# Performance work log

Hardware: AMD Instinct MI355X
Metric: run time of the kernel (lower is better)

The kernel has to match this reference:

```python
import jax, jax.numpy as jnp
import numpy as np

B, H, S, D = 1, 16, 4096, 64

def setup_inputs() -> dict:
    key = jax.random.key(0)
    k1, k2, k3 = jax.random.split(key, 3)
    query = jax.random.normal(k1, (B, H, S, D), dtype=jnp.float32)
    key_t = jax.random.normal(k2, (B, H, S, D), dtype=jnp.float32)
    value = jax.random.normal(k3, (B, H, S, D), dtype=jnp.float32)
    attn_mask = jnp.zeros((B, 1, S, S), dtype=jnp.float32)
    return {"query": query, "key": key_t, "value": value, "attn_mask": attn_mask}

def reference(query, key, value, attn_mask):
    d = query.shape[-1]
    # [B,H,S,S] = QK^T / sqrt(d) + mask
    scores = jnp.einsum("bhqd,bhkd->bhqk", query, key) / jnp.sqrt(jnp.float32(d))
    scores = scores + attn_mask
    probs = jax.nn.softmax(scores, axis=-1)
    # dropout_p = 0.0 -> identity
    out = jnp.einsum("bhqk,bhkd->bhqd", probs, value)
    return out
```

## Files before the change

kernel.cpp:

```cpp
#include <hip/hip_runtime.h>
#include <stdint.h>

#define LOG2E  1.44269504088896f
#define QSCALE (0.125f * LOG2E)

typedef float    f32x4_t  __attribute__((ext_vector_type(4)));
typedef float    f32x16_t __attribute__((ext_vector_type(16)));
typedef _Float16 f16x8_t  __attribute__((ext_vector_type(8)));
typedef _Float16 f16x2_t  __attribute__((ext_vector_type(2)));

#if __has_builtin(__builtin_amdgcn_exp2f)
#define EXP2F(x) __builtin_amdgcn_exp2f(x)
#else
#define EXP2F(x) exp2f(x)
#endif

__device__ __forceinline__ float rowsum2(f16x2_t p, float acc) {
#if __has_builtin(__builtin_amdgcn_fdot2)
  return __builtin_amdgcn_fdot2(p, (f16x2_t){(_Float16)1.0f, (_Float16)1.0f}, acc, false);
#else
  return acc + (float)p[0] + (float)p[1];
#endif
}

__global__ void prep_kernel(const float* __restrict__ M, const float* __restrict__ K,
                            const float* __restrict__ V, _Float16* __restrict__ Kh,
                            _Float16* __restrict__ Vth, int* __restrict__ flag) {
  __shared__ __align__(16) _Float16 T[64 * 72];
  const int tid = threadIdx.x;
  const int bid = blockIdx.x;

  {
    const float* p = M + (size_t)bid * 8192 + (size_t)tid * 4;
    unsigned acc = 0;
#pragma unroll
    for (int i = 0; i < 8; ++i) {
      f32x4_t v = *(const f32x4_t*)(p + (size_t)i * 1024);
      acc |= __float_as_uint(v[0]) | __float_as_uint(v[1]) |
             __float_as_uint(v[2]) | __float_as_uint(v[3]);
    }
    if (acc & 0x7fffffffu) atomicOr(flag, 1);
  }

  if (Kh != nullptr) {
    {
      const size_t idx = ((size_t)bid * 256 + tid) * 8;
      f32x4_t a = *(const f32x4_t*)(K + idx);
      f32x4_t b = *(const f32x4_t*)(K + idx + 4);
      union { _Float16 h[8]; uint4 q; } U;
#pragma unroll
      for (int j = 0; j < 4; ++j) { U.h[j] = (_Float16)a[j]; U.h[4 + j] = (_Float16)b[j]; }
      *(uint4*)(Kh + idx) = U.q;
    }
    if (bid < 1024) {
      const int head = bid >> 6;
      const int st   = bid & 63;
      const size_t hoff = (size_t)head * 4096 * 64;
      const int sl    = tid >> 2;
      const int fbase = (tid & 3) * 16;
      const float* src = V + hoff + (size_t)(st * 64 + sl) * 64 + fbase;
#pragma unroll
      for (int c = 0; c < 4; ++c) {
        f32x4_t a = *(const f32x4_t*)(src + c * 4);
#pragma unroll
        for (int j = 0; j < 4; ++j) T[(fbase + c * 4 + j) * 72 + sl] = (_Float16)a[j];
      }
      __syncthreads();
      const int feat = tid >> 2;
      const int sb   = (tid & 3) * 16;
      uint4 r0 = *(const uint4*)&T[feat * 72 + sb];
      uint4 r1 = *(const uint4*)&T[feat * 72 + sb + 8];
      _Float16* dst = Vth + hoff + (size_t)feat * 4096 + st * 64 + sb;
      *(uint4*)(dst)     = r0;
      *(uint4*)(dst + 8) = r1;
    }
  }
}

template <bool WS16, bool SPLIT>
__launch_bounds__(256, SPLIT ? 4 : 2)
__global__ void sdpa_kernel(const float* __restrict__ Qg, const float* __restrict__ Kg,
                            const float* __restrict__ Vg, const float* __restrict__ Mg,
                            const _Float16* __restrict__ Kh, const _Float16* __restrict__ Vth,
                            float* __restrict__ Og, float* __restrict__ Opart,
                            float* __restrict__ Lpart, const int* __restrict__ flag) {
  __shared__ __align__(16) _Float16 Ks[64 * 72];
  __shared__ __align__(16) _Float16 Vt[64 * 72];

  const int tid  = threadIdx.x;
  const int bid  = blockIdx.x;
  const int hh   = ((bid & 7) << 1) | ((bid >> 3) & 1);
  const int half = SPLIT ? ((bid >> 4) & 1) : 0;
  const int qt   = SPLIT ? (bid >> 5) : (bid >> 4);
  const int w    = tid >> 6;
  const int lane = tid & 63;
  const int n    = lane & 31;
  const int h2   = lane >> 5;
  const int sig  = (n & 0x13) | ((n >> 1) & 4) | ((n << 1) & 8);
  const bool has_mask = (*flag) != 0;

  const size_t hoff = (size_t)hh * 4096 * 64;
  const int qcol = qt * 128 + w * 32 + n;
  const int ktlo = half * 32;
  const int ktn  = SPLIT ? 32 : 64;

  f16x8_t qf[4];
  {
    const float* qp = Qg + hoff + (size_t)qcol * 64 + 8 * h2;
#pragma unroll
    for (int kh = 0; kh < 4; ++kh) {
      f32x4_t a = *(const f32x4_t*)(qp + kh * 16);
      f32x4_t b = *(const f32x4_t*)(qp + kh * 16 + 4);
      union { _Float16 h[8]; f16x8_t v; } U;
#pragma unroll
      for (int j = 0; j < 4; ++j) { U.h[j] = (_Float16)(a[j] * QSCALE); U.h[4 + j] = (_Float16)(b[j] * QSCALE); }
      qf[kh] = U.v;
    }
  }

  f32x16_t o0 = {0.f,0.f,0.f,0.f,0.f,0.f,0.f,0.f,0.f,0.f,0.f,0.f,0.f,0.f,0.f,0.f};
  f32x16_t o1 = o0;
  float lacc = 0.0f;

#pragma unroll 1
  for (int kk = 0; kk < ktn; ++kk) {
    const int kt    = ktlo + kk;
    const int kbase = kt * 64;

    uint4 kk0, kk1, vv0, vv1;
    f32x4_t k0, k1, k2, k3;
    float vlo[8], vhi[8];
    if (WS16) {
      const _Float16* kp = Kh + hoff + (size_t)(kbase + (tid >> 2)) * 64 + (tid & 3) * 16;
      kk0 = *(const uint4*)(kp);
      kk1 = *(const uint4*)(kp + 8);
      const _Float16* vp = Vth + hoff + (size_t)(tid >> 2) * 4096 + kbase + (tid & 3) * 16;
      vv0 = *(const uint4*)(vp);
      vv1 = *(const uint4*)(vp + 8);
    } else {
      const float* kp = Kg + hoff + (size_t)(kbase + (tid >> 2)) * 64 + (tid & 3) * 16;
      k0 = *(const f32x4_t*)(kp + 0);
      k1 = *(const f32x4_t*)(kp + 4);
      k2 = *(const f32x4_t*)(kp + 8);
      k3 = *(const f32x4_t*)(kp + 12);
      const float* vp = Vg + hoff + (size_t)(kbase + (tid >> 5) * 8) * 64 + (tid & 31);
#pragma unroll
      for (int j = 0; j < 8; ++j) {
        vlo[j] = vp[(size_t)j * 64];
        vhi[j] = vp[(size_t)j * 64 + 32];
      }
    }

    f32x4_t mk[2][2][2];
    if (has_mask) {
      const float* mp = Mg + (size_t)qcol * 4096 + kbase + 8 * h2;
#pragma unroll
      for (int kb = 0; kb < 2; ++kb)
#pragma unroll
        for (int a = 0; a < 2; ++a)
#pragma unroll
          for (int b = 0; b < 2; ++b)
            mk[kb][a][b] = *(const f32x4_t*)(mp + kb * 32 + 16 * a + 4 * b);
    }

    __syncthreads();

    if (WS16) {
      *(uint4*)&Ks[(tid >> 2) * 72 + (tid & 3) * 16]     = kk0;
      *(uint4*)&Ks[(tid >> 2) * 72 + (tid & 3) * 16 + 8] = kk1;
      *(uint4*)&Vt[(tid >> 2) * 72 + (tid & 3) * 16]     = vv0;
      *(uint4*)&Vt[(tid >> 2) * 72 + (tid & 3) * 16 + 8] = vv1;
    } else {
      union { _Float16 h[8]; uint4 q; } A, B;
#pragma unroll
      for (int j = 0; j < 4; ++j) {
        A.h[j] = (_Float16)k0[j];  A.h[4 + j] = (_Float16)k1[j];
        B.h[j] = (_Float16)k2[j];  B.h[4 + j] = (_Float16)k3[j];
      }
      *(uint4*)&Ks[(tid >> 2) * 72 + (tid & 3) * 16]     = A.q;
      *(uint4*)&Ks[(tid >> 2) * 72 + (tid & 3) * 16 + 8] = B.q;
      union { _Float16 h[8]; uint4 q; } C, D;
#pragma unroll
      for (int j = 0; j < 8; ++j) { C.h[j] = (_Float16)vlo[j]; D.h[j] = (_Float16)vhi[j]; }
      *(uint4*)&Vt[(tid & 31) * 72 + (tid >> 5) * 8]        = C.q;
      *(uint4*)&Vt[((tid & 31) + 32) * 72 + (tid >> 5) * 8] = D.q;
    }

    __syncthreads();

#pragma unroll
    for (int kb = 0; kb < 2; ++kb) {
      f32x16_t acc = {0.f,0.f,0.f,0.f,0.f,0.f,0.f,0.f,0.f,0.f,0.f,0.f,0.f,0.f,0.f,0.f};
#pragma unroll
      for (int kh = 0; kh < 4; ++kh) {
        const f16x8_t ka = *(const f16x8_t*)&Ks[(kb * 32 + sig) * 72 + kh * 16 + 8 * h2];
        acc = __builtin_amdgcn_mfma_f32_32x32x16_f16(ka, qf[kh], acc, 0, 0, 0);
      }
#pragma unroll
      for (int a = 0; a < 2; ++a) {
        union { _Float16 h[8]; f16x8_t v; f16x2_t p2[4]; } F;
#pragma unroll
        for (int idx = 0; idx < 8; ++idx) {
          float x = acc[8 * a + idx];
          if (has_mask) x = __builtin_fmaf(mk[kb][a][idx >> 2][idx & 3], LOG2E, x);
          F.h[idx] = (_Float16)EXP2F(x);
        }
#pragma unroll
        for (int t = 0; t < 4; ++t) lacc = rowsum2(F.p2[t], lacc);
        const int f = kb * 2 + a;
        const f16x8_t v0 = *(const f16x8_t*)&Vt[n * 72 + f * 16 + 8 * h2];
        o0 = __builtin_amdgcn_mfma_f32_32x32x16_f16(F.v, v0, o0, 0, 0, 0);
        const f16x8_t v1 = *(const f16x8_t*)&Vt[(32 + n) * 72 + f * 16 + 8 * h2];
        o1 = __builtin_amdgcn_mfma_f32_32x32x16_f16(F.v, v1, o1, 0, 0, 0);
      }
    }
  }

  float lq = lacc + __shfl_xor(lacc, 32);
  if constexpr (SPLIT) {
    float* op = Opart + (size_t)half * (16 * 4096 * 64) + hoff;
#pragma unroll
    for (int r2 = 0; r2 < 4; ++r2) {
#pragma unroll
      for (int rr = 0; rr < 4; ++rr) {
        const int reg  = r2 * 4 + rr;
        const int qrow = rr + 8 * r2 + 4 * h2;
        const size_t row = (size_t)(qt * 128 + w * 32 + qrow) * 64;
        op[row + n]      = o0[reg];
        op[row + 32 + n] = o1[reg];
      }
    }
    if (h2 == 0)
      Lpart[(size_t)half * 65536 + (size_t)hh * 4096 + qcol] = lq;
  } else {
    float* op = Og + hoff;
#pragma unroll
    for (int r2 = 0; r2 < 4; ++r2) {
#pragma unroll
      for (int rr = 0; rr < 4; ++rr) {
        const int reg  = r2 * 4 + rr;
        const int qrow = rr + 8 * r2 + 4 * h2;
        float lr  = __shfl(lq, qrow);
        float inv = 1.0f / lr;
        const size_t row = (size_t)(qt * 128 + w * 32 + qrow) * 64;
        op[row + n]      = o0[reg] * inv;
        op[row + 32 + n] = o1[reg] * inv;
      }
    }
  }
}

__global__ void combine_kernel(const float* __restrict__ Opart, const float* __restrict__ Lpart,
                               float* __restrict__ Og) {
  const size_t e   = ((size_t)blockIdx.x * 256 + threadIdx.x) * 8;
  const size_t row = e >> 6;
  const float inv = 1.0f / (Lpart[row] + Lpart[65536 + row]);
  const float* a = Opart + e;
  const float* b = Opart + (size_t)16 * 4096 * 64 + e;
  f32x4_t x0 = *(const f32x4_t*)a,      x1 = *(const f32x4_t*)(a + 4);
  f32x4_t y0 = *(const f32x4_t*)b,      y1 = *(const f32x4_t*)(b + 4);
  f32x4_t r0, r1;
#pragma unroll
  for (int j = 0; j < 4; ++j) { r0[j] = (x0[j] + y0[j]) * inv; r1[j] = (x1[j] + y1[j]) * inv; }
  *(f32x4_t*)(Og + e)     = r0;
  *(f32x4_t*)(Og + e + 4) = r1;
}

extern "C" void kernel_launch(void* const* d_in, const int* in_sizes, int n_in,
                              void* d_out, int out_size, void* d_ws, size_t ws_size,
                              hipStream_t stream) {
  const float* Q = (const float*)d_in[0];
  const float* K = (const float*)d_in[1];
  const float* V = (const float*)d_in[2];
  const float* M = (const float*)d_in[3];
  float* O = (float*)d_out;

  const size_t NELEM = (size_t)16 * 4096 * 64;
  const size_t need16    = 256 + 2 * NELEM * sizeof(_Float16);
  const size_t needsplit = need16 + 2 * NELEM * sizeof(float)
                                  + 2 * (size_t)65536 * sizeof(float);
  int* flag = (int*)d_ws;
  const bool ws16  = (ws_size >= need16);
  const bool split = (ws_size >= needsplit);
  _Float16* Kh    = ws16 ? (_Float16*)((char*)d_ws + 256) : nullptr;
  _Float16* Vth   = ws16 ? Kh + NELEM : nullptr;
  float*    Opart = split ? (float*)(Vth + NELEM) : nullptr;
  float*    Lpart = split ? Opart + 2 * NELEM : nullptr;

  hipMemsetAsync(flag, 0, sizeof(int), stream);
  prep_kernel<<<2048, 256, 0, stream>>>(M, K, V, Kh, Vth, flag);

  if (split) {
    sdpa_kernel<true, true><<<1024, 256, 0, stream>>>(Q, K, V, M, Kh, Vth, O, Opart, Lpart, flag);
    combine_kernel<<<2048, 256, 0, stream>>>(Opart, Lpart, O);
  } else if (ws16) {
    sdpa_kernel<true, false><<<512, 256, 0, stream>>>(Q, K, V, M, Kh, Vth, O, nullptr, nullptr, flag);
  } else {
    sdpa_kernel<false, false><<<512, 256, 0, stream>>>(Q, K, V, M, nullptr, nullptr, O, nullptr, nullptr, flag);
  }
}
```

Baseline: 238.2 us.

## Double-buffer K/V shared tiles and prefetch next tile during MFMA compute

Splits the K/V shared-memory tiles into two buffers. The next tile's global loads are issued before the current tile's compute and written to the other buffer afterwards, which cuts one barrier per iteration and hides load latency behind the MFMAs. It also wraps the MFMA sections in s_setprio so waves doing matrix work get issue priority. The cost is double the LDS footprint and more live registers across the compute, which may reduce occupancy.

```diff
diff --git a/kernel.cpp b/kernel.cpp
--- a/kernel.cpp
+++ b/kernel.cpp
@@ -21,6 +21,66 @@
 #else
   return acc + (float)p[0] + (float)p[1];
 #endif
+}
+
+struct SRegs {
+  uint4 kk0, kk1, vv0, vv1;
+  f32x4_t k0, k1, k2, k3;
+  float vlo[8], vhi[8];
+};
+
+template <bool WS16>
+__device__ __forceinline__ void stage_load(SRegs& r, int tid, size_t hoff, int kbase,
+                                           const _Float16* __restrict__ Kh,
+                                           const _Float16* __restrict__ Vth,
+                                           const float* __restrict__ Kg,
+                                           const float* __restrict__ Vg) {
+  if constexpr (WS16) {
+    const _Float16* kp = Kh + hoff + (size_t)(kbase + (tid >> 2)) * 64 + (tid & 3) * 16;
+    r.kk0 = *(const uint4*)(kp);
+    r.kk1 = *(const uint4*)(kp + 8);
+    const _Float16* vp = Vth + hoff + (size_t)(tid >> 2) * 4096 + kbase + (tid & 3) * 16;
+    r.vv0 = *(const uint4*)(vp);
+    r.vv1 = *(const uint4*)(vp + 8);
+  } else {
+    const float* kp = Kg + hoff + (size_t)(kbase + (tid >> 2)) * 64 + (tid & 3) * 16;
+    r.k0 = *(const f32x4_t*)(kp + 0);
+    r.k1 = *(const f32x4_t*)(kp + 4);
+    r.k2 = *(const f32x4_t*)(kp + 8);
+    r.k3 = *(const f32x4_t*)(kp + 12);
+    const float* vp = Vg + hoff + (size_t)(kbase + (tid >> 5) * 8) * 64 + (tid & 31);
+#pragma unroll
+    for (int j = 0; j < 8; ++j) {
+      r.vlo[j] = vp[(size_t)j * 64];
+      r.vhi[j] = vp[(size_t)j * 64 + 32];
+    }
+  }
+}
+
+template <bool WS16>
+__device__ __forceinline__ void stage_write(const SRegs& r, int tid,
+                                            _Float16* __restrict__ Ksb,
+                                            _Float16* __restrict__ Vtb) {
+  if constexpr (WS16) {
+    *(uint4*)&Ksb[(tid >> 2) * 72 + (tid & 3) * 16]     = r.kk0;
+    *(uint4*)&Ksb[(tid >> 2) * 72 + (tid & 3) * 16 + 8] = r.kk1;
+    *(uint4*)&Vtb[(tid >> 2) * 72 + (tid & 3) * 16]     = r.vv0;
+    *(uint4*)&Vtb[(tid >> 2) * 72 + (tid & 3) * 16 + 8] = r.vv1;
+  } else {
+    union { _Float16 h[8]; uint4 q; } A, B;
+#pragma unroll
+    for (int j = 0; j < 4; ++j) {
+      A.h[j] = (_Float16)r.k0[j];  A.h[4 + j] = (_Float16)r.k1[j];
+      B.h[j] = (_Float16)r.k2[j];  B.h[4 + j] = (_Float16)r.k3[j];
+    }
+    *(uint4*)&Ksb[(tid >> 2) * 72 + (tid & 3) * 16]     = A.q;
+    *(uint4*)&Ksb[(tid >> 2) * 72 + (tid & 3) * 16 + 8] = B.q;
+    union { _Float16 h[8]; uint4 q; } C, D;
+#pragma unroll
+    for (int j = 0; j < 8; ++j) { C.h[j] = (_Float16)r.vlo[j]; D.h[j] = (_Float16)r.vhi[j]; }
+    *(uint4*)&Vtb[(tid & 31) * 72 + (tid >> 5) * 8]        = C.q;
+    *(uint4*)&Vtb[((tid & 31) + 32) * 72 + (tid >> 5) * 8] = D.q;
+  }
 }
 
 __global__ void prep_kernel(const float* __restrict__ M, const float* __restrict__ K,
@@ -84,8 +144,8 @@
                             const _Float16* __restrict__ Kh, const _Float16* __restrict__ Vth,
                             float* __restrict__ Og, float* __restrict__ Opart,
                             float* __restrict__ Lpart, const int* __restrict__ flag) {
-  __shared__ __align__(16) _Float16 Ks[64 * 72];
-  __shared__ __align__(16) _Float16 Vt[64 * 72];
+  __shared__ __align__(16) _Float16 Ks[2][64 * 72];
+  __shared__ __align__(16) _Float16 Vt[2][64 * 72];
 
   const int tid  = threadIdx.x;
   const int bid  = blockIdx.x;
@@ -122,34 +182,20 @@
   f32x16_t o1 = o0;
   float lacc = 0.0f;
 
+  SRegs r;
+  stage_load<WS16>(r, tid, hoff, ktlo * 64, Kh, Vth, Kg, Vg);
+  stage_write<WS16>(r, tid, &Ks[0][0], &Vt[0][0]);
+  __syncthreads();
+
 #pragma unroll 1
   for (int kk = 0; kk < ktn; ++kk) {
-    const int kt    = ktlo + kk;
-    const int kbase = kt * 64;
-
-    uint4 kk0, kk1, vv0, vv1;
-    f32x4_t k0, k1, k2, k3;
-    float vlo[8], vhi[8];
-    if (WS16) {
-      const _Float16* kp = Kh + hoff + (size_t)(kbase + (tid >> 2)) * 64 + (tid & 3) * 16;
-      kk0 = *(const uint4*)(kp);
-      kk1 = *(const uint4*)(kp + 8);
-      const _Float16* vp = Vth + hoff + (size_t)(tid >> 2) * 4096 + kbase + (tid & 3) * 16;
-      vv0 = *(const uint4*)(vp);
-      vv1 = *(const uint4*)(vp + 8);
-    } else {
-      const float* kp = Kg + hoff + (size_t)(kbase + (tid >> 2)) * 64 + (tid & 3) * 16;
-      k0 = *(const f32x4_t*)(kp + 0);
-      k1 = *(const f32x4_t*)(kp + 4);
-      k2 = *(const f32x4_t*)(kp + 8);
-      k3 = *(const f32x4_t*)(kp + 12);
-      const float* vp = Vg + hoff + (size_t)(kbase + (tid >> 5) * 8) * 64 + (tid & 31);
-#pragma unroll
-      for (int j = 0; j < 8; ++j) {
-        vlo[j] = vp[(size_t)j * 64];
-        vhi[j] = vp[(size_t)j * 64 + 32];
-      }
-    }
+    const int kbase = (ktlo + kk) * 64;
+    _Float16* const Ksc = &Ks[kk & 1][0];
+    _Float16* const Vtc = &Vt[kk & 1][0];
+    _Float16* const Ksn = &Ks[(kk & 1) ^ 1][0];
+    _Float16* const Vtn = &Vt[(kk & 1) ^ 1][0];
+
+    if (kk < ktn - 1) stage_load<WS16>(r, tid, hoff, kbase + 64, Kh, Vth, Kg, Vg);
 
     f32x4_t mk[2][2][2];
     if (has_mask) {
@@ -163,39 +209,16 @@
             mk[kb][a][b] = *(const f32x4_t*)(mp + kb * 32 + 16 * a + 4 * b);
     }
 
-    __syncthreads();
-
-    if (WS16) {
-      *(uint4*)&Ks[(tid >> 2) * 72 + (tid & 3) * 16]     = kk0;
-      *(uint4*)&Ks[(tid >> 2) * 72 + (tid & 3) * 16 + 8] = kk1;
-      *(uint4*)&Vt[(tid >> 2) * 72 + (tid & 3) * 16]     = vv0;
-      *(uint4*)&Vt[(tid >> 2) * 72 + (tid & 3) * 16 + 8] = vv1;
-    } else {
-      union { _Float16 h[8]; uint4 q; } A, B;
-#pragma unroll
-      for (int j = 0; j < 4; ++j) {
-        A.h[j] = (_Float16)k0[j];  A.h[4 + j] = (_Float16)k1[j];
-        B.h[j] = (_Float16)k2[j];  B.h[4 + j] = (_Float16)k3[j];
-      }
-      *(uint4*)&Ks[(tid >> 2) * 72 + (tid & 3) * 16]     = A.q;
-      *(uint4*)&Ks[(tid >> 2) * 72 + (tid & 3) * 16 + 8] = B.q;
-      union { _Float16 h[8]; uint4 q; } C, D;
-#pragma unroll
-      for (int j = 0; j < 8; ++j) { C.h[j] = (_Float16)vlo[j]; D.h[j] = (_Float16)vhi[j]; }
-      *(uint4*)&Vt[(tid & 31) * 72 + (tid >> 5) * 8]        = C.q;
-      *(uint4*)&Vt[((tid & 31) + 32) * 72 + (tid >> 5) * 8] = D.q;
-    }
-
-    __syncthreads();
-
 #pragma unroll
     for (int kb = 0; kb < 2; ++kb) {
       f32x16_t acc = {0.f,0.f,0.f,0.f,0.f,0.f,0.f,0.f,0.f,0.f,0.f,0.f,0.f,0.f,0.f,0.f};
+      __builtin_amdgcn_s_setprio(1);
 #pragma unroll
       for (int kh = 0; kh < 4; ++kh) {
-        const f16x8_t ka = *(const f16x8_t*)&Ks[(kb * 32 + sig) * 72 + kh * 16 + 8 * h2];
+        const f16x8_t ka = *(const f16x8_t*)&Ksc[(kb * 32 + sig) * 72 + kh * 16 + 8 * h2];
         acc = __builtin_amdgcn_mfma_f32_32x32x16_f16(ka, qf[kh], acc, 0, 0, 0);
       }
+      __builtin_amdgcn_s_setprio(0);
 #pragma unroll
       for (int a = 0; a < 2; ++a) {
         union { _Float16 h[8]; f16x8_t v; f16x2_t p2[4]; } F;
@@ -208,11 +231,18 @@
 #pragma unroll
         for (int t = 0; t < 4; ++t) lacc = rowsum2(F.p2[t], lacc);
         const int f = kb * 2 + a;
-        const f16x8_t v0 = *(const f16x8_t*)&Vt[n * 72 + f * 16 + 8 * h2];
+        const f16x8_t v0 = *(const f16x8_t*)&Vtc[n * 72 + f * 16 + 8 * h2];
+        const f16x8_t v1 = *(const f16x8_t*)&Vtc[(32 + n) * 72 + f * 16 + 8 * h2];
+        __builtin_amdgcn_s_setprio(1);
         o0 = __builtin_amdgcn_mfma_f32_32x32x16_f16(F.v, v0, o0, 0, 0, 0);
-        const f16x8_t v1 = *(const f16x8_t*)&Vt[(32 + n) * 72 + f * 16 + 8 * h2];
         o1 = __builtin_amdgcn_mfma_f32_32x32x16_f16(F.v, v1, o1, 0, 0, 0);
-      }
+        __builtin_amdgcn_s_setprio(0);
+      }
+    }
+
+    if (kk < ktn - 1) {
+      stage_write<WS16>(r, tid, Ksn, Vtn);
+      __syncthreads();
     }
   }
 
```

Result: slower. 298.5 us (+25.3%).

## Double-buffer K/V shared-memory tiles and prefetch next tile during compute

Applied to the files above, without the earlier changes.

Splits the K and V shared-memory tiles into two buffers. The global loads for the next key tile are issued before the current tile's MFMA and softmax work, and written into the alternate buffer afterward, so each iteration needs one barrier instead of two. The aim is to hide global-memory latency behind compute. In exchange, shared-memory use per block doubles and the prefetched values stay live in registers across the compute phase, which could reduce occupancy against the 4- and 2-block launch bounds.

```diff
diff --git a/kernel.cpp b/kernel.cpp
--- a/kernel.cpp
+++ b/kernel.cpp
@@ -77,6 +77,50 @@
   }
 }
 
+#define STAGE_LOAD(KB)                                                                   \
+  if constexpr (WS16) {                                                                  \
+    const _Float16* kp = Kh + hoff + (size_t)((KB) + (tid >> 2)) * 64 + (tid & 3) * 16;  \
+    kk0 = *(const uint4*)(kp);                                                           \
+    kk1 = *(const uint4*)(kp + 8);                                                       \
+    const _Float16* vp = Vth + hoff + (size_t)(tid >> 2) * 4096 + (KB) + (tid & 3) * 16; \
+    vv0 = *(const uint4*)(vp);                                                           \
+    vv1 = *(const uint4*)(vp + 8);                                                       \
+  } else {                                                                               \
+    const float* kp = Kg + hoff + (size_t)((KB) + (tid >> 2)) * 64 + (tid & 3) * 16;     \
+    k0 = *(const f32x4_t*)(kp + 0);                                                      \
+    k1 = *(const f32x4_t*)(kp + 4);                                                      \
+    k2 = *(const f32x4_t*)(kp + 8);                                                      \
+    k3 = *(const f32x4_t*)(kp + 12);                                                     \
+    const float* vp = Vg + hoff + (size_t)((KB) + (tid >> 5) * 8) * 64 + (tid & 31);     \
+    _Pragma("unroll")                                                                    \
+    for (int j = 0; j < 8; ++j) {                                                        \
+      vlo[j] = vp[(size_t)j * 64];                                                       \
+      vhi[j] = vp[(size_t)j * 64 + 32];                                                  \
+    }                                                                                    \
+  }
+
+#define STAGE_WRITE(KSB, VTB)                                                            \
+  if constexpr (WS16) {                                                                  \
+    *(uint4*)&(KSB)[(tid >> 2) * 72 + (tid & 3) * 16]     = kk0;                         \
+    *(uint4*)&(KSB)[(tid >> 2) * 72 + (tid & 3) * 16 + 8] = kk1;                         \
+    *(uint4*)&(VTB)[(tid >> 2) * 72 + (tid & 3) * 16]     = vv0;                         \
+    *(uint4*)&(VTB)[(tid >> 2) * 72 + (tid & 3) * 16 + 8] = vv1;                         \
+  } else {                                                                               \
+    union { _Float16 h[8]; uint4 q; } A, B;                                              \
+    _Pragma("unroll")                                                                    \
+    for (int j = 0; j < 4; ++j) {                                                        \
+      A.h[j] = (_Float16)k0[j];  A.h[4 + j] = (_Float16)k1[j];                           \
+      B.h[j] = (_Float16)k2[j];  B.h[4 + j] = (_Float16)k3[j];                           \
+    }                                                                                    \
+    *(uint4*)&(KSB)[(tid >> 2) * 72 + (tid & 3) * 16]     = A.q;                         \
+    *(uint4*)&(KSB)[(tid >> 2) * 72 + (tid & 3) * 16 + 8] = B.q;                         \
+    union { _Float16 h[8]; uint4 q; } C, D;                                              \
+    _Pragma("unroll")                                                                    \
+    for (int j = 0; j < 8; ++j) { C.h[j] = (_Float16)vlo[j]; D.h[j] = (_Float16)vhi[j]; }\
+    *(uint4*)&(VTB)[(tid & 31) * 72 + (tid >> 5) * 8]        = C.q;                      \
+    *(uint4*)&(VTB)[((tid & 31) + 32) * 72 + (tid >> 5) * 8] = D.q;                      \
+  }
+
 template <bool WS16, bool SPLIT>
 __launch_bounds__(256, SPLIT ? 4 : 2)
 __global__ void sdpa_kernel(const float* __restrict__ Qg, const float* __restrict__ Kg,
@@ -84,8 +128,8 @@
                             const _Float16* __restrict__ Kh, const _Float16* __restrict__ Vth,
                             float* __restrict__ Og, float* __restrict__ Opart,
                             float* __restrict__ Lpart, const int* __restrict__ flag) {
-  __shared__ __align__(16) _Float16 Ks[64 * 72];
-  __shared__ __align__(16) _Float16 Vt[64 * 72];
+  __shared__ __align__(16) _Float16 Ks[2][64 * 72];
+  __shared__ __align__(16) _Float16 Vt[2][64 * 72];
 
   const int tid  = threadIdx.x;
   const int bid  = blockIdx.x;
@@ -122,33 +166,21 @@
   f32x16_t o1 = o0;
   float lacc = 0.0f;
 
+  uint4 kk0, kk1, vv0, vv1;
+  f32x4_t k0, k1, k2, k3;
+  float vlo[8], vhi[8];
+
+  STAGE_LOAD(ktlo * 64)
+  STAGE_WRITE(Ks[0], Vt[0])
+  __syncthreads();
+
 #pragma unroll 1
   for (int kk = 0; kk < ktn; ++kk) {
-    const int kt    = ktlo + kk;
-    const int kbase = kt * 64;
-
-    uint4 kk0, kk1, vv0, vv1;
-    f32x4_t k0, k1, k2, k3;
-    float vlo[8], vhi[8];
-    if (WS16) {
-      const _Float16* kp = Kh + hoff + (size_t)(kbase + (tid >> 2)) * 64 + (tid & 3) * 16;
-      kk0 = *(const uint4*)(kp);
-      kk1 = *(const uint4*)(kp + 8);
-      const _Float16* vp = Vth + hoff + (size_t)(tid >> 2) * 4096 + kbase + (tid & 3) * 16;
-      vv0 = *(const uint4*)(vp);
-      vv1 = *(const uint4*)(vp + 8);
-    } else {
-      const float* kp = Kg + hoff + (size_t)(kbase + (tid >> 2)) * 64 + (tid & 3) * 16;
-      k0 = *(const f32x4_t*)(kp + 0);
-      k1 = *(const f32x4_t*)(kp + 4);
-      k2 = *(const f32x4_t*)(kp + 8);
-      k3 = *(const f32x4_t*)(kp + 12);
-      const float* vp = Vg + hoff + (size_t)(kbase + (tid >> 5) * 8) * 64 + (tid & 31);
-#pragma unroll
-      for (int j = 0; j < 8; ++j) {
-        vlo[j] = vp[(size_t)j * 64];
-        vhi[j] = vp[(size_t)j * 64 + 32];
-      }
+    const int kbase = (ktlo + kk) * 64;
+    const int cur   = kk & 1;
+
+    if (kk + 1 < ktn) {
+      STAGE_LOAD(kbase + 64)
     }
 
     f32x4_t mk[2][2][2];
@@ -163,37 +195,12 @@
             mk[kb][a][b] = *(const f32x4_t*)(mp + kb * 32 + 16 * a + 4 * b);
     }
 
-    __syncthreads();
-
-    if (WS16) {
-      *(uint4*)&Ks[(tid >> 2) * 72 + (tid & 3) * 16]     = kk0;
-      *(uint4*)&Ks[(tid >> 2) * 72 + (tid & 3) * 16 + 8] = kk1;
-      *(uint4*)&Vt[(tid >> 2) * 72 + (tid & 3) * 16]     = vv0;
-      *(uint4*)&Vt[(tid >> 2) * 72 + (tid & 3) * 16 + 8] = vv1;
-    } else {
-      union { _Float16 h[8]; uint4 q; } A, B;
-#pragma unroll
-      for (int j = 0; j < 4; ++j) {
-        A.h[j] = (_Float16)k0[j];  A.h[4 + j] = (_Float16)k1[j];
-        B.h[j] = (_Float16)k2[j];  B.h[4 + j] = (_Float16)k3[j];
-      }
-      *(uint4*)&Ks[(tid >> 2) * 72 + (tid & 3) * 16]     = A.q;
-      *(uint4*)&Ks[(tid >> 2) * 72 + (tid & 3) * 16 + 8] = B.q;
-      union { _Float16 h[8]; uint4 q; } C, D;
-#pragma unroll
-      for (int j = 0; j < 8; ++j) { C.h[j] = (_Float16)vlo[j]; D.h[j] = (_Float16)vhi[j]; }
-      *(uint4*)&Vt[(tid & 31) * 72 + (tid >> 5) * 8]        = C.q;
-      *(uint4*)&Vt[((tid & 31) + 32) * 72 + (tid >> 5) * 8] = D.q;
-    }
-
-    __syncthreads();
-
 #pragma unroll
     for (int kb = 0; kb < 2; ++kb) {
       f32x16_t acc = {0.f,0.f,0.f,0.f,0.f,0.f,0.f,0.f,0.f,0.f,0.f,0.f,0.f,0.f,0.f,0.f};
 #pragma unroll
       for (int kh = 0; kh < 4; ++kh) {
-        const f16x8_t ka = *(const f16x8_t*)&Ks[(kb * 32 + sig) * 72 + kh * 16 + 8 * h2];
+        const f16x8_t ka = *(const f16x8_t*)&Ks[cur][(kb * 32 + sig) * 72 + kh * 16 + 8 * h2];
         acc = __builtin_amdgcn_mfma_f32_32x32x16_f16(ka, qf[kh], acc, 0, 0, 0);
       }
 #pragma unroll
@@ -208,11 +215,16 @@
 #pragma unroll
         for (int t = 0; t < 4; ++t) lacc = rowsum2(F.p2[t], lacc);
         const int f = kb * 2 + a;
-        const f16x8_t v0 = *(const f16x8_t*)&Vt[n * 72 + f * 16 + 8 * h2];
+        const f16x8_t v0 = *(const f16x8_t*)&Vt[cur][n * 72 + f * 16 + 8 * h2];
         o0 = __builtin_amdgcn_mfma_f32_32x32x16_f16(F.v, v0, o0, 0, 0, 0);
-        const f16x8_t v1 = *(const f16x8_t*)&Vt[(32 + n) * 72 + f * 16 + 8 * h2];
+        const f16x8_t v1 = *(const f16x8_t*)&Vt[cur][(32 + n) * 72 + f * 16 + 8 * h2];
         o1 = __builtin_amdgcn_mfma_f32_32x32x16_f16(F.v, v1, o1, 0, 0, 0);
       }
+    }
+
+    if (kk + 1 < ktn) {
+      STAGE_WRITE(Ks[cur ^ 1], Vt[cur ^ 1])
+      __syncthreads();
     }
   }
 
```

Measured after the change: 256.0 us. 7.5% more time.
